# Optimization experiments

Hardware: AMD Instinct MI355X
Metric: run time of the kernel (lower is better)

Reference implementation:

```python
import jax, jax.numpy as jnp
import numpy as np

# Constants mirroring MS / MultiLayers_MS forward args (scalars closed over)
HEADS = 8
BETA = 0.5          # GAT_MS_2_3 init arg 'beta' (mean-shift coordinate gate strength)
T = 1.0             # temperature 't' forward arg
BAND_WIDTH = 1.0    # 'band_width' forward arg
MAX_ITER = 3        # 'max_iter' forward arg (iterative mean-shift steps)
SELF_DISTANCE = 0.01  # 'self_distance' forward arg: distance assigned to the diagonal
USE_STD_ATT = False # 'use_std_att' forward arg
NEG_INF = -1e9


def setup_inputs() -> dict:
    key = jax.random.key(0)
    ks = jax.random.split(key, 16)
    N, D = 3072, 256
    x = jax.random.normal(ks[0], (N, D), dtype=jnp.float32)
    xyz = jax.random.normal(ks[1], (N, 3), dtype=jnp.float32) * 3.0
    # delta_y = |y_hat - y_hat^T| as produced by GAT_Classifier (detached)
    y_hat = jax.random.uniform(ks[2], (N, 1), dtype=jnp.float32)
    delta_y = jnp.abs(y_hat - y_hat.T)
    distance_mask = jax.random.uniform(ks[3], (N, N)) < 0.3   # sparse pairwise gate
    big_inter_mask = jax.random.uniform(ks[4], (N, N)) < 0.9  # inter-chain gate
    s = 1.0 / np.sqrt(D)  # ~ xavier_uniform scale for D x D
    def lin_w(k):
        return jax.random.uniform(k, (D, D), jnp.float32, minval=-s, maxval=s)
    Wq, Wk, Wv, Wo = lin_w(ks[5]), lin_w(ks[6]), lin_w(ks[7]), lin_w(ks[8])
    z = jnp.zeros((D,), jnp.float32)
    return dict(x=x, xyz=xyz, delta_y=delta_y,
                distance_mask=distance_mask, big_inter_mask=big_inter_mask,
                Wq=Wq, bq=z, Wk=Wk, bk=z, Wv=Wv, bv=z, Wo=Wo, bo=z)


def _mean_shift(xyz, q, k, v, delta_y, valid):
    """Iterative distance/band-masked multi-head attention (mean_shift).
    q,k,v: [N,H,Dh]; delta_y: [N,N]; valid: [N,N] bool. Returns (xyz, feat [N,D])."""
    N, H, Dh = q.shape
    eye = jnp.eye(N, dtype=bool)
    # content scores, computed once (q,k fixed across iterations)
    scores = jnp.einsum('nhd,mhd->hnm', q, k) / jnp.sqrt(jnp.float32(Dh))  # [H,N,N]
    if USE_STD_ATT:
        mu = scores.mean(axis=-1, keepdims=True)
        sd = scores.std(axis=-1, keepdims=True)
        scores = (scores - mu) / (sd + 1e-5)
    inv2bw2 = 1.0 / (2.0 * BAND_WIDTH * BAND_WIDTH)
    feat = None
    for _ in range(MAX_ITER):
        # pairwise squared distances of current coordinates [N,N]
        d2 = jnp.sum((xyz[:, None, :] - xyz[None, :, :]) ** 2, axis=-1)
        d2 = jnp.where(eye, SELF_DISTANCE ** 2, d2)
        # banded logits: content score, Gaussian distance band, prediction-difference gate
        logits = T * scores - BETA * (d2 * inv2bw2) - delta_y  # [H,N,N]
        logits = jnp.where(valid, logits, NEG_INF)
        attn = jax.nn.softmax(logits, axis=-1)                 # [H,N,N]
        xyz = attn.mean(axis=0) @ xyz                          # mean-shift coords [N,3]
        feat = jnp.einsum('hnm,mhd->nhd', attn, v).reshape(N, H * Dh)
    return xyz, feat


def reference(x, xyz, delta_y, distance_mask, big_inter_mask,
              Wq, bq, Wk, bk, Wv, bv, Wo, bo):
    N, D = x.shape
    H, Dh = HEADS, D // HEADS
    q = (x @ Wq + bq).reshape(N, H, Dh)
    k = (x @ Wk + bk).reshape(N, H, Dh)
    v = (x @ Wv + bv).reshape(N, H, Dh)
    eye = jnp.eye(N, dtype=bool)
    valid = (distance_mask & big_inter_mask) | eye  # keep self to avoid empty rows
    xyz_out, feat = _mean_shift(xyz, q, k, v, delta_y, valid)
    out = feat @ Wo + bo + x   # out_proj + residual (MS.forward)
    return xyz_out, out
```

## Files before the change

### kernel.cpp

```cpp
#include <hip/hip_runtime.h>
#include <hip/hip_fp16.h>

#define NN 3072
#define DD 256
#define NH 8
#define SPLIT 4
#define KT (NN / SPLIT / 64)
#define NKT2 (NN / 64)
#define VHALF ((NN / 16) * 256)
#define LN2INV 1.4426950408889634f

typedef _Float16 h16;
typedef __attribute__((ext_vector_type(4))) _Float16 half4;
typedef __attribute__((ext_vector_type(8))) _Float16 half8;
typedef __attribute__((ext_vector_type(4))) float f32x4;

#if __has_builtin(__builtin_amdgcn_exp2f)
#define EXP2(x) __builtin_amdgcn_exp2f(x)
#else
#define EXP2(x) __expf((x) * 0.69314718056f)
#endif

#define MFMA16(a, b, c) __builtin_amdgcn_mfma_f32_16x16x16f16(a, b, c, 0, 0, 0)

__device__ __forceinline__ void async16(const h16* g, h16* l, int lane) {
#if __has_builtin(__builtin_amdgcn_global_load_lds)
  __builtin_amdgcn_global_load_lds(
      (const __attribute__((address_space(1))) void*)(g + (size_t)lane * 8),
      (__attribute__((address_space(3))) void*)l, 16, 0, 0);
#else
  *(half8*)(l + lane * 8) = *(const half8*)(g + (size_t)lane * 8);
#endif
}

__device__ inline void write_aug(int q, float x, float y, float z,
                                 h16* __restrict__ qaug, h16* __restrict__ kaug,
                                 h16* __restrict__ xzT3) {
  float sx = 0.5f * LN2INV * x, sy = 0.5f * LN2INV * y, sz = 0.5f * LN2INV * z;
  h16 shx = (h16)sx, shy = (h16)sy, shz = (h16)sz;
  h16 slx = (h16)(sx - (float)shx), sly = (h16)(sy - (float)shy), slz = (h16)(sz - (float)shz);
  h16 hx = (h16)x, hy = (h16)y, hz = (h16)z;
  h16 lx = (h16)(x - (float)hx), ly = (h16)(y - (float)hy), lz = (h16)(z - (float)hz);
  float n2n = -0.25f * LN2INV * (x * x + y * y + z * z);
  h16 nh = (h16)n2n, nl = (h16)(n2n - (float)nh);
  h16 qa[16], ka[16];
  #pragma unroll
  for (int i = 0; i < 16; ++i) { qa[i] = (h16)0.f; ka[i] = (h16)0.f; }
  qa[0] = shx; qa[1] = shy; qa[2] = shz;
  qa[3] = shx; qa[4] = shy; qa[5] = shz;
  qa[6] = slx; qa[7] = sly; qa[8] = slz;
  qa[9] = (h16)1.f; qa[10] = (h16)1.f;
  qa[11] = (h16)n2n;
  ka[0] = hx; ka[1] = hy; ka[2] = hz;
  ka[3] = lx; ka[4] = ly; ka[5] = lz;
  ka[6] = hx; ka[7] = hy; ka[8] = hz;
  ka[9] = nh; ka[10] = nl;
  ka[11] = (h16)1.f;
  *(half8*)(qaug + (size_t)q * 16) = ((half8*)qa)[0];
  *(half8*)(qaug + (size_t)q * 16 + 8) = ((half8*)qa)[1];
  *(half8*)(kaug + (size_t)q * 16) = ((half8*)ka)[0];
  *(half8*)(kaug + (size_t)q * 16 + 8) = ((half8*)ka)[1];
  int kt2 = q >> 6, kk = q & 63;
  int f = kk >> 4, qd = (kk >> 2) & 3, j = kk & 3;
  h16* b = xzT3 + ((size_t)kt2 << 10) + f * 256 + qd * 64 + j;
  b[0] = (h16)1.f;
  b[4] = hx; b[8] = hy; b[12] = hz;
  b[16] = lx; b[20] = ly; b[24] = lz;
  #pragma unroll
  for (int m = 7; m < 16; ++m) b[m * 4] = (h16)0.f;
}

__global__ __launch_bounds__(256) void k_convert(
    const float* __restrict__ x, const float* __restrict__ xyz,
    h16* __restrict__ xb, h16* __restrict__ qaug,
    h16* __restrict__ kaug, h16* __restrict__ xzT3,
    float* __restrict__ numT) {
  int t = blockIdx.x * 256 + threadIdx.x;
  const int NX = NN * DD;
  if (t < NX) { xb[t] = (h16)x[t]; numT[t] = 0.f; return; }
  int q = t - NX;
  if (q < NN) write_aug(q, xyz[q * 3], xyz[q * 3 + 1], xyz[q * 3 + 2], qaug, kaug, xzT3);
}

__global__ __launch_bounds__(256) void k_wt(
    const float* __restrict__ Wq, const float* __restrict__ Wk,
    const float* __restrict__ Wv, const float* __restrict__ Wo,
    h16* __restrict__ wtq, h16* __restrict__ wtk, h16* __restrict__ wtv,
    h16* __restrict__ wto) {
  __shared__ float tile[32][33];
  int m = blockIdx.z;
  const float* W = (m == 0) ? Wq : (m == 1) ? Wk : (m == 2) ? Wv : Wo;
  h16* wt = (m == 0) ? wtq : (m == 1) ? wtk : (m == 2) ? wtv : wto;
  int n0 = blockIdx.x * 32, k0 = blockIdx.y * 32;
  int tx = threadIdx.x & 31, ty = threadIdx.x >> 5;
  #pragma unroll
  for (int i = 0; i < 4; ++i)
    tile[ty + i * 8][tx] = W[(size_t)(k0 + ty + i * 8) * 256 + n0 + tx];
  __syncthreads();
  #pragma unroll
  for (int i = 0; i < 4; ++i)
    wt[(size_t)(n0 + ty + i * 8) * 256 + k0 + tx] = (h16)tile[tx][ty + i * 8];
}

__global__ __launch_bounds__(256) void k_prep(
    const float* __restrict__ dy, const int* __restrict__ dm,
    const int* __restrict__ bim, h16* __restrict__ dynT3) {
  __shared__ h16 sv[16][1036];
  int qt = blockIdx.y;
  int cb = blockIdx.x;
  int t = threadIdx.x;
  int c0 = cb * 1024 + t * 4;
  #pragma unroll
  for (int r = 0; r < 16; ++r) {
    int row = qt * 16 + r;
    size_t idx = (size_t)row * NN + c0;
    int4 m4 = *(const int4*)(dm + idx);
    int4 b4 = *(const int4*)(bim + idx);
    float4 d4 = *(const float4*)(dy + idx);
    h16* s = &sv[r][t * 4];
    int mm[4] = {m4.x & b4.x, m4.y & b4.y, m4.z & b4.z, m4.w & b4.w};
    float dd[4] = {d4.x, d4.y, d4.z, d4.w};
    #pragma unroll
    for (int j = 0; j < 4; ++j) {
      bool diag = (row == c0 + j);
      bool valid = (mm[j] != 0) | diag;
      s[j] = (h16)(valid ? (-LN2INV * (dd[j] + (diag ? 2.5e-5f : 0.f))) : -43281.f);
    }
  }
  __syncthreads();
  #pragma unroll
  for (int s2 = 0; s2 < 8; ++s2) {
    int s = t + s2 * 256;
    int tile = s >> 7;
    int sl = s & 127;
    int chunk = sl >> 6;
    int lane = sl & 63;
    int row = lane & 15, quad = lane >> 4;
    int base = tile * 64 + chunk * 32 + quad * 4;
    half4 lo = *(const half4*)&sv[row][base];
    half4 hi = *(const half4*)&sv[row][base + 16];
    half8 o;
    #pragma unroll
    for (int j = 0; j < 4; ++j) { o[j] = lo[j]; o[j + 4] = hi[j]; }
    h16* dst = dynT3 + (((size_t)qt * NKT2 + (cb * 16 + tile)) << 10) + sl * 8;
    *(half8*)dst = o;
  }
}

__device__ inline void gemm_body(const h16* __restrict__ A, const h16* __restrict__ Bt,
                                 const float* __restrict__ bias, void* __restrict__ out,
                                 const float* __restrict__ resid, int M, int mode,
                                 float scale, int bx, int by) {
  int lane = threadIdx.x & 63;
  int wave = threadIdx.x >> 6;
  int col = lane & 15, quad = lane >> 4;
  int m0 = bx * 32;
  int n0 = by * 64 + wave * 16;
  f32x4 acc[2];
  acc[0] = (f32x4){0.f, 0.f, 0.f, 0.f};
  acc[1] = (f32x4){0.f, 0.f, 0.f, 0.f};
  #pragma unroll
  for (int kk = 0; kk < DD; kk += 32) {
    half8 b = *(const half8*)(Bt + (size_t)(n0 + col) * DD + kk + quad * 8);
    #pragma unroll
    for (int mr = 0; mr < 2; ++mr) {
      half8 a = *(const half8*)(A + (size_t)(m0 + mr * 16 + col) * DD + kk + quad * 8);
      acc[mr] = __builtin_amdgcn_mfma_f32_16x16x32_f16(a, b, acc[mr], 0, 0, 0);
    }
  }
  float bb = bias[n0 + col];
  #pragma unroll
  for (int mr = 0; mr < 2; ++mr) {
    #pragma unroll
    for (int r = 0; r < 4; ++r) {
      int m = m0 + mr * 16 + quad * 4 + r;
      int n = n0 + col;
      float v = acc[mr][r] + bb;
      if (mode == 0)      ((h16*)out)[(size_t)m * DD + n] = (h16)(v * scale);
      else if (mode == 3) ((h16*)out)[((size_t)(n >> 5) * NN + m) * 32 + (n & 31)] = (h16)v;
      else if (mode == 4) {
        int hh = n >> 5, d = n & 31;
        size_t a = ((((size_t)hh * 2 + (d >> 4)) * (NN / 16) + (m >> 4)) * 64 +
                    ((m >> 2) & 3) * 16 + (d & 15)) * 4 + (m & 3);
        ((h16*)out)[a] = (h16)v;
      }
      else ((float*)out)[(size_t)m * DD + n] = v + resid[(size_t)m * DD + n];
    }
  }
}

__global__ __launch_bounds__(256) void k_gemm(
    const h16* __restrict__ A, const h16* __restrict__ Bt,
    const float* __restrict__ bias, void* __restrict__ out,
    const float* __restrict__ resid, int M, int mode, float scale) {
  gemm_body(A, Bt, bias, out, resid, M, mode, scale, blockIdx.x, blockIdx.y);
}

__global__ __launch_bounds__(256) void k_gemm3(
    const h16* __restrict__ A, const h16* __restrict__ wtq,
    const h16* __restrict__ wtk, const h16* __restrict__ wtv,
    const float* __restrict__ bq, const float* __restrict__ bk,
    const float* __restrict__ bv, h16* __restrict__ qb, h16* __restrict__ kbh,
    h16* __restrict__ vA, float qscale) {
  int z = blockIdx.z;
  const h16* Bt = (z == 0) ? wtq : (z == 1) ? wtk : wtv;
  const float* bias = (z == 0) ? bq : (z == 1) ? bk : bv;
  void* out = (z == 0) ? (void*)qb : (z == 1) ? (void*)kbh : (void*)vA;
  int mode = (z == 0) ? 0 : (z == 1) ? 3 : 4;
  gemm_body(A, Bt, bias, out, nullptr, NN, mode, (z == 0) ? qscale : 1.f,
            blockIdx.x, blockIdx.y);
}

__device__ __forceinline__ void stage_tile(int h, int lane, int qt, int kt2,
                                           const h16* __restrict__ dynT3,
                                           const h16* __restrict__ kaug,
                                           const h16* __restrict__ xzT3,
                                           h16* bdy, h16* bka, h16* bxz) {
  if (h < 2)
    async16(dynT3 + (((size_t)qt * NKT2 + kt2) << 10) + h * 512, bdy + h * 512, lane);
  else if (h < 4)
    async16(kaug + ((size_t)kt2 << 10) + (h - 2) * 512, bka + (h - 2) * 512, lane);
  else if (h < 6)
    async16(xzT3 + ((size_t)kt2 << 10) + (h - 4) * 512, bxz + (h - 4) * 512, lane);
}

__device__ __forceinline__ void ldkf(const h16* __restrict__ kbh_h, int k0,
                                     int col, int quad, half8 kf[4]) {
  #pragma unroll
  for (int f = 0; f < 4; ++f)
    kf[f] = *(const half8*)(kbh_h + (size_t)(k0 + f * 16 + col) * 32 + quad * 8);
}

template <int LAST>
__device__ __forceinline__ void ms_compute(
    const h16* __restrict__ bdy, const h16* __restrict__ bka,
    const h16* __restrict__ bxz, const half8 kf[4], half8 qaf, half8 qf,
    const h16* __restrict__ vA0, int lane, int col, int quad,
    f32x4& accS, f32x4& fc0, f32x4& fc1) {
  half8 kz = {};
  half8 dv0 = *(const half8*)(bdy + lane * 8);
  half8 dv1 = *(const half8*)(bdy + 512 + lane * 8);
  #pragma unroll
  for (int f = 0; f < 4; ++f) {
    half8 ka = (quad < 2) ? *(const half8*)(bka + (f * 16 + col) * 16 + quad * 8) : kz;
    half8 dv = (f & 2) ? dv1 : dv0;
    f32x4 cc;
    #pragma unroll
    for (int r = 0; r < 4; ++r) cc[r] = (float)dv[(f & 1) * 4 + r];
    f32x4 g = __builtin_amdgcn_mfma_f32_16x16x32_f16(ka, qaf, cc, 0, 0, 0);
    f32x4 s = __builtin_amdgcn_mfma_f32_16x16x32_f16(kf[f], qf, g, 0, 0, 0);
    half4 pv;
    #pragma unroll
    for (int r = 0; r < 4; ++r) pv[r] = (h16)EXP2(s[r]);
    half4 xa = *(const half4*)(bxz + f * 256 + lane * 4);
    accS = MFMA16(xa, pv, accS);
    if (LAST) {
      half4 v0 = *(const half4*)(vA0 + f * 256 + lane * 4);
      half4 v1 = *(const half4*)(vA0 + VHALF + f * 256 + lane * 4);
      fc0 = MFMA16(v0, pv, fc0);
      fc1 = MFMA16(v1, pv, fc1);
    }
  }
}

template <int LAST>
__global__ __launch_bounds__(512, 4) void k_msattn(
    const h16* __restrict__ qb, const h16* __restrict__ kbh,
    const h16* __restrict__ vA, const h16* __restrict__ dynT3,
    const h16* __restrict__ qaug, const h16* __restrict__ kaug,
    const h16* __restrict__ xzT3, float* __restrict__ den_s,
    float* __restrict__ axh_s, float* __restrict__ axl_s,
    float* __restrict__ numT) {
  __shared__ h16 s_dy[2][1024];
  __shared__ h16 s_ka[2][1024];
  __shared__ h16 s_xz[2][1024];
  const int tid = threadIdx.x;
  const int h = tid >> 6;
  const int lane = tid & 63;
  const int col = lane & 15;
  const int quad = lane >> 4;
  const int qt = blockIdx.x;
  const int q0 = qt * 16;
  const int tb = blockIdx.y * KT;

  half8 kz = {};
  half8 qf = *(const half8*)(qb + (size_t)(q0 + col) * DD + h * 32 + quad * 8);
  half8 qaf = (quad < 2) ? *(const half8*)(qaug + (size_t)(q0 + col) * 16 + quad * 8) : kz;
  const h16* kbh_h = kbh + (size_t)h * NN * 32;
  const h16* vb = vA + (size_t)h * 2 * (NN / 16) * 256;
  f32x4 accS = (f32x4){0.f, 0.f, 0.f, 0.f};
  f32x4 fc0 = (f32x4){0.f, 0.f, 0.f, 0.f};
  f32x4 fc1 = (f32x4){0.f, 0.f, 0.f, 0.f};
  half8 kfA[4], kfB[4];

  stage_tile(h, lane, qt, tb, dynT3, kaug, xzT3, s_dy[0], s_ka[0], s_xz[0]);
  ldkf(kbh_h, tb * 64, col, quad, kfA);
  __syncthreads();
  #pragma unroll 1
  for (int kt = 0; kt < KT; kt += 2) {
    int t1 = tb + kt + 1;
    stage_tile(h, lane, qt, t1, dynT3, kaug, xzT3, s_dy[1], s_ka[1], s_xz[1]);
    ldkf(kbh_h, t1 * 64, col, quad, kfB);
    ms_compute<LAST>(s_dy[0], s_ka[0], s_xz[0], kfA, qaf, qf,
                     vb + (size_t)(tb + kt) * 1024,
                     lane, col, quad, accS, fc0, fc1);
    __syncthreads();
    int t2 = (kt + 2 < KT) ? tb + kt + 2 : t1;
    if (kt + 2 < KT)
      stage_tile(h, lane, qt, t2, dynT3, kaug, xzT3, s_dy[0], s_ka[0], s_xz[0]);
    ldkf(kbh_h, t2 * 64, col, quad, kfA);
    ms_compute<LAST>(s_dy[1], s_ka[1], s_xz[1], kfB, qaf, qf,
                     vb + (size_t)t1 * 1024,
                     lane, col, quad, accS, fc0, fc1);
    __syncthreads();
  }

  int q = q0 + col;
  size_t sidx = (size_t)(blockIdx.y * NH + h) * NN + q;
  if (quad == 0) {
    den_s[sidx] = accS[0];
    axh_s[sidx * 3 + 0] = accS[1];
    axh_s[sidx * 3 + 1] = accS[2];
    axh_s[sidx * 3 + 2] = accS[3];
  } else if (quad == 1) {
    axl_s[sidx * 3 + 0] = accS[0];
    axl_s[sidx * 3 + 1] = accS[1];
    axl_s[sidx * 3 + 2] = accS[2];
  }
  if (LAST) {
    #pragma unroll
    for (int r = 0; r < 4; ++r) {
      atomicAdd(&numT[(size_t)(h * 32 + quad * 4 + r) * NN + q], fc0[r]);
      atomicAdd(&numT[(size_t)(h * 32 + 16 + quad * 4 + r) * NN + q], fc1[r]);
    }
  }
}

__global__ __launch_bounds__(256) void k_combine(
    const float* __restrict__ den_s, const float* __restrict__ axh_s,
    const float* __restrict__ axl_s, float* __restrict__ den_tot,
    h16* __restrict__ qaug, h16* __restrict__ kaug, h16* __restrict__ xzT3,
    float* __restrict__ out3) {
  int h = threadIdx.x & 7;
  int q = blockIdx.x * 32 + (threadIdx.x >> 3);
  float d = 0.f, x = 0.f, y = 0.f, z = 0.f;
  #pragma unroll
  for (int s = 0; s < SPLIT; ++s) {
    size_t idx = (size_t)(s * NH + h) * NN + q;
    d += den_s[idx];
    x += axh_s[idx * 3 + 0] + axl_s[idx * 3 + 0];
    y += axh_s[idx * 3 + 1] + axl_s[idx * 3 + 1];
    z += axh_s[idx * 3 + 2] + axl_s[idx * 3 + 2];
  }
  den_tot[h * NN + q] = d;
  float inv = 0.125f / d;
  float X = x * inv, Y = y * inv, Z = z * inv;
  #pragma unroll
  for (int m = 1; m < 8; m <<= 1) {
    X += __shfl_xor(X, m);
    Y += __shfl_xor(Y, m);
    Z += __shfl_xor(Z, m);
  }
  if (h == 0) {
    if (out3) {
      out3[q * 3 + 0] = X;
      out3[q * 3 + 1] = Y;
      out3[q * 3 + 2] = Z;
    } else {
      write_aug(q, X, Y, Z, qaug, kaug, xzT3);
    }
  }
}

__global__ __launch_bounds__(256) void k_finish(
    const float* __restrict__ numT, const float* __restrict__ den_tot,
    h16* __restrict__ featb) {
  __shared__ float tile[32][33];
  int q0 = blockIdx.x * 32, d0 = blockIdx.y * 32;
  int tx = threadIdx.x & 31, ty = threadIdx.x >> 5;
  #pragma unroll
  for (int i = 0; i < 4; ++i)
    tile[ty + i * 8][tx] = numT[(size_t)(d0 + ty + i * 8) * NN + q0 + tx];
  __syncthreads();
  int h = d0 >> 5;
  #pragma unroll
  for (int i = 0; i < 4; ++i) {
    int q = q0 + ty + i * 8;
    float inv = 1.f / den_tot[h * NN + q];
    featb[(size_t)q * DD + d0 + tx] = (h16)(tile[tx][ty + i * 8] * inv);
  }
}

extern "C" void kernel_launch(void* const* d_in, const int* in_sizes, int n_in,
                              void* d_out, int out_size, void* d_ws, size_t ws_size,
                              hipStream_t stream) {
  const float* x   = (const float*)d_in[0];
  const float* xyz = (const float*)d_in[1];
  const float* dy  = (const float*)d_in[2];
  const int* dm    = (const int*)d_in[3];
  const int* bim   = (const int*)d_in[4];
  const float* Wq = (const float*)d_in[5];
  const float* bq = (const float*)d_in[6];
  const float* Wk = (const float*)d_in[7];
  const float* bk = (const float*)d_in[8];
  const float* Wv = (const float*)d_in[9];
  const float* bv = (const float*)d_in[10];
  const float* Wo = (const float*)d_in[11];
  const float* bo = (const float*)d_in[12];

  char* p = (char*)d_ws;
  h16* xb  = (h16*)p; p += (size_t)NN * DD * 2;
  h16* wtq = (h16*)p; p += 256 * 256 * 2;
  h16* wtk = (h16*)p; p += 256 * 256 * 2;
  h16* wtv = (h16*)p; p += 256 * 256 * 2;
  h16* wto = (h16*)p; p += 256 * 256 * 2;
  h16* qb    = (h16*)p; p += (size_t)NN * DD * 2;
  h16* kbh   = (h16*)p; p += (size_t)NN * DD * 2;
  h16* vA    = (h16*)p; p += (size_t)NN * DD * 2;
  h16* featb = (h16*)p; p += (size_t)NN * DD * 2;
  h16* dynT3 = (h16*)p; p += (size_t)NN * NN * 2;
  h16* qaug  = (h16*)p; p += (size_t)NN * 16 * 2;
  h16* kaug  = (h16*)p; p += (size_t)NN * 16 * 2;
  h16* xzT3  = (h16*)p; p += (size_t)NKT2 * 1024 * 2;
  float* den_s = (float*)p; p += (size_t)SPLIT * NH * NN * 4;
  float* axh_s = (float*)p; p += (size_t)SPLIT * NH * NN * 3 * 4;
  float* axl_s = (float*)p; p += (size_t)SPLIT * NH * NN * 3 * 4;
  float* den_tot = (float*)p; p += (size_t)NH * NN * 4;
  float* numT = (float*)p; p += (size_t)DD * NN * 4;

  k_convert<<<(NN * DD + NN + 255) / 256, 256, 0, stream>>>(x, xyz, xb, qaug,
                                                            kaug, xzT3, numT);
  k_wt<<<dim3(8, 8, 4), 256, 0, stream>>>(Wq, Wk, Wv, Wo, wtq, wtk, wtv, wto);
  k_prep<<<dim3(3, 192), 256, 0, stream>>>(dy, dm, bim, dynT3);
  k_gemm3<<<dim3(96, 4, 3), 256, 0, stream>>>(xb, wtq, wtk, wtv, bq, bk, bv,
                                              qb, kbh, vA,
                                              0.17677669529663689f * LN2INV);

  float* xyz_final = (float*)d_out;
  float* out_final = (float*)d_out + NN * 3;

  k_msattn<0><<<dim3(NN / 16, SPLIT), 512, 0, stream>>>(
      qb, kbh, vA, dynT3, qaug, kaug, xzT3, den_s, axh_s, axl_s, nullptr);
  k_combine<<<96, 256, 0, stream>>>(den_s, axh_s, axl_s, den_tot,
                                    qaug, kaug, xzT3, nullptr);
  k_msattn<0><<<dim3(NN / 16, SPLIT), 512, 0, stream>>>(
      qb, kbh, vA, dynT3, qaug, kaug, xzT3, den_s, axh_s, axl_s, nullptr);
  k_combine<<<96, 256, 0, stream>>>(den_s, axh_s, axl_s, den_tot,
                                    qaug, kaug, xzT3, nullptr);
  k_msattn<1><<<dim3(NN / 16, SPLIT), 512, 0, stream>>>(
      qb, kbh, vA, dynT3, qaug, kaug, xzT3, den_s, axh_s, axl_s, numT);
  k_combine<<<96, 256, 0, stream>>>(den_s, axh_s, axl_s, den_tot,
                                    nullptr, nullptr, nullptr, xyz_final);
  k_finish<<<dim3(96, 8), 256, 0, stream>>>(numT, den_tot, featb);
  k_gemm<<<dim3(96, 4), 256, 0, stream>>>(featb, wto, bo, out_final, x, NN, 2, 1.f);
}
```

Baseline: 320.3 us.

## Merge preprocessing kernels into one launch and stagger attention block start

Fuses the three preprocessing kernels (fp16 conversion/aug setup, weight transposes, mask/delta packing) into a single launch that dispatches on block index range, cutting two kernel launches and their gaps. It also makes each attention block sleep in proportion to its linear block index divided by 256, staggering when blocks start. The staggering is meant to spread out the memory traffic at kernel start, but it delays later blocks and may add idle time.

```diff
diff --git a/kernel.cpp b/kernel.cpp
--- a/kernel.cpp
+++ b/kernel.cpp
@@ -9,6 +9,9 @@
 #define NKT2 (NN / 64)
 #define VHALF ((NN / 16) * 256)
 #define LN2INV 1.4426950408889634f
+#define PREP_BLKS 576
+#define CONV_BLKS ((NN * DD + NN) / 256)
+#define WT_BLKS 256
 
 typedef _Float16 h16;
 typedef __attribute__((ext_vector_type(4))) _Float16 half4;
@@ -70,80 +73,78 @@
   for (int m = 7; m < 16; ++m) b[m * 4] = (h16)0.f;
 }
 
-__global__ __launch_bounds__(256) void k_convert(
+__global__ __launch_bounds__(256) void k_pre(
     const float* __restrict__ x, const float* __restrict__ xyz,
-    h16* __restrict__ xb, h16* __restrict__ qaug,
-    h16* __restrict__ kaug, h16* __restrict__ xzT3,
-    float* __restrict__ numT) {
-  int t = blockIdx.x * 256 + threadIdx.x;
-  const int NX = NN * DD;
-  if (t < NX) { xb[t] = (h16)x[t]; numT[t] = 0.f; return; }
-  int q = t - NX;
-  if (q < NN) write_aug(q, xyz[q * 3], xyz[q * 3 + 1], xyz[q * 3 + 2], qaug, kaug, xzT3);
-}
-
-__global__ __launch_bounds__(256) void k_wt(
+    const float* __restrict__ dy, const int* __restrict__ dm,
+    const int* __restrict__ bim,
     const float* __restrict__ Wq, const float* __restrict__ Wk,
     const float* __restrict__ Wv, const float* __restrict__ Wo,
+    h16* __restrict__ xb, h16* __restrict__ qaug, h16* __restrict__ kaug,
+    h16* __restrict__ xzT3, float* __restrict__ numT,
     h16* __restrict__ wtq, h16* __restrict__ wtk, h16* __restrict__ wtv,
-    h16* __restrict__ wto) {
-  __shared__ float tile[32][33];
-  int m = blockIdx.z;
-  const float* W = (m == 0) ? Wq : (m == 1) ? Wk : (m == 2) ? Wv : Wo;
-  h16* wt = (m == 0) ? wtq : (m == 1) ? wtk : (m == 2) ? wtv : wto;
-  int n0 = blockIdx.x * 32, k0 = blockIdx.y * 32;
-  int tx = threadIdx.x & 31, ty = threadIdx.x >> 5;
-  #pragma unroll
-  for (int i = 0; i < 4; ++i)
-    tile[ty + i * 8][tx] = W[(size_t)(k0 + ty + i * 8) * 256 + n0 + tx];
-  __syncthreads();
-  #pragma unroll
-  for (int i = 0; i < 4; ++i)
-    wt[(size_t)(n0 + ty + i * 8) * 256 + k0 + tx] = (h16)tile[tx][ty + i * 8];
-}
-
-__global__ __launch_bounds__(256) void k_prep(
-    const float* __restrict__ dy, const int* __restrict__ dm,
-    const int* __restrict__ bim, h16* __restrict__ dynT3) {
+    h16* __restrict__ wto, h16* __restrict__ dynT3) {
   __shared__ h16 sv[16][1036];
-  int qt = blockIdx.y;
-  int cb = blockIdx.x;
+  int b = blockIdx.x;
   int t = threadIdx.x;
-  int c0 = cb * 1024 + t * 4;
-  #pragma unroll
-  for (int r = 0; r < 16; ++r) {
-    int row = qt * 16 + r;
-    size_t idx = (size_t)row * NN + c0;
-    int4 m4 = *(const int4*)(dm + idx);
-    int4 b4 = *(const int4*)(bim + idx);
-    float4 d4 = *(const float4*)(dy + idx);
-    h16* s = &sv[r][t * 4];
-    int mm[4] = {m4.x & b4.x, m4.y & b4.y, m4.z & b4.z, m4.w & b4.w};
-    float dd[4] = {d4.x, d4.y, d4.z, d4.w};
-    #pragma unroll
-    for (int j = 0; j < 4; ++j) {
-      bool diag = (row == c0 + j);
-      bool valid = (mm[j] != 0) | diag;
-      s[j] = (h16)(valid ? (-LN2INV * (dd[j] + (diag ? 2.5e-5f : 0.f))) : -43281.f);
-    }
-  }
-  __syncthreads();
-  #pragma unroll
-  for (int s2 = 0; s2 < 8; ++s2) {
-    int s = t + s2 * 256;
-    int tile = s >> 7;
-    int sl = s & 127;
-    int chunk = sl >> 6;
-    int lane = sl & 63;
-    int row = lane & 15, quad = lane >> 4;
-    int base = tile * 64 + chunk * 32 + quad * 4;
-    half4 lo = *(const half4*)&sv[row][base];
-    half4 hi = *(const half4*)&sv[row][base + 16];
-    half8 o;
-    #pragma unroll
-    for (int j = 0; j < 4; ++j) { o[j] = lo[j]; o[j + 4] = hi[j]; }
-    h16* dst = dynT3 + (((size_t)qt * NKT2 + (cb * 16 + tile)) << 10) + sl * 8;
-    *(half8*)dst = o;
+  if (b < PREP_BLKS) {
+    int cb = b % 3, qt = b / 3;
+    int c0 = cb * 1024 + t * 4;
+    #pragma unroll
+    for (int r = 0; r < 16; ++r) {
+      int row = qt * 16 + r;
+      size_t idx = (size_t)row * NN + c0;
+      int4 m4 = *(const int4*)(dm + idx);
+      int4 b4 = *(const int4*)(bim + idx);
+      float4 d4 = *(const float4*)(dy + idx);
+      h16* s = &sv[r][t * 4];
+      int mm[4] = {m4.x & b4.x, m4.y & b4.y, m4.z & b4.z, m4.w & b4.w};
+      float dd[4] = {d4.x, d4.y, d4.z, d4.w};
+      #pragma unroll
+      for (int j = 0; j < 4; ++j) {
+        bool diag = (row == c0 + j);
+        bool valid = (mm[j] != 0) | diag;
+        s[j] = (h16)(valid ? (-LN2INV * (dd[j] + (diag ? 2.5e-5f : 0.f))) : -43281.f);
+      }
+    }
+    __syncthreads();
+    #pragma unroll
+    for (int s2 = 0; s2 < 8; ++s2) {
+      int s = t + s2 * 256;
+      int tile = s >> 7;
+      int sl = s & 127;
+      int lane = sl & 63;
+      int row = lane & 15, quad = lane >> 4;
+      int base = tile * 64 + (sl >> 6) * 32 + quad * 4;
+      half4 lo = *(const half4*)&sv[row][base];
+      half4 hi = *(const half4*)&sv[row][base + 16];
+      half8 o;
+      #pragma unroll
+      for (int j = 0; j < 4; ++j) { o[j] = lo[j]; o[j + 4] = hi[j]; }
+      h16* dst = dynT3 + (((size_t)qt * NKT2 + (cb * 16 + tile)) << 10) + sl * 8;
+      *(half8*)dst = o;
+    }
+  } else if (b < PREP_BLKS + CONV_BLKS) {
+    int u = (b - PREP_BLKS) * 256 + t;
+    const int NX = NN * DD;
+    if (u < NX) { xb[u] = (h16)x[u]; numT[u] = 0.f; return; }
+    int q = u - NX;
+    if (q < NN)
+      write_aug(q, xyz[q * 3], xyz[q * 3 + 1], xyz[q * 3 + 2], qaug, kaug, xzT3);
+  } else {
+    float* tf = (float*)sv;
+    int w = b - PREP_BLKS - CONV_BLKS;
+    int m = w >> 6;
+    int n0 = (w & 7) * 32, k0 = ((w >> 3) & 7) * 32;
+    const float* W = (m == 0) ? Wq : (m == 1) ? Wk : (m == 2) ? Wv : Wo;
+    h16* wt = (m == 0) ? wtq : (m == 1) ? wtk : (m == 2) ? wtv : wto;
+    int tx = t & 31, ty = t >> 5;
+    #pragma unroll
+    for (int i = 0; i < 4; ++i)
+      tf[(ty + i * 8) * 33 + tx] = W[(size_t)(k0 + ty + i * 8) * 256 + n0 + tx];
+    __syncthreads();
+    #pragma unroll
+    for (int i = 0; i < 4; ++i)
+      wt[(size_t)(n0 + ty + i * 8) * 256 + k0 + tx] = (h16)tf[tx * 33 + ty + i * 8];
   }
 }
 
@@ -282,6 +283,12 @@
   const int qt = blockIdx.x;
   const int q0 = qt * 16;
   const int tb = blockIdx.y * KT;
+
+  int phase = (blockIdx.x + gridDim.x * blockIdx.y) >> 8;
+  for (int i = 0; i < phase; ++i) {
+    __builtin_amdgcn_s_sleep(16);
+    __builtin_amdgcn_s_sleep(16);
+  }
 
   half8 kz = {};
   half8 qf = *(const half8*)(qb + (size_t)(q0 + col) * DD + h * 32 + quad * 8);
@@ -428,10 +435,9 @@
   float* den_tot = (float*)p; p += (size_t)NH * NN * 4;
   float* numT = (float*)p; p += (size_t)DD * NN * 4;
 
-  k_convert<<<(NN * DD + NN + 255) / 256, 256, 0, stream>>>(x, xyz, xb, qaug,
-                                                            kaug, xzT3, numT);
-  k_wt<<<dim3(8, 8, 4), 256, 0, stream>>>(Wq, Wk, Wv, Wo, wtq, wtk, wtv, wto);
-  k_prep<<<dim3(3, 192), 256, 0, stream>>>(dy, dm, bim, dynT3);
+  k_pre<<<PREP_BLKS + CONV_BLKS + WT_BLKS, 256, 0, stream>>>(
+      x, xyz, dy, dm, bim, Wq, Wk, Wv, Wo,
+      xb, qaug, kaug, xzT3, numT, wtq, wtk, wtv, wto, dynT3);
   k_gemm3<<<dim3(96, 4, 3), 256, 0, stream>>>(xb, wtq, wtk, wtv, bq, bk, bv,
                                               qb, kbh, vA,
                                               0.17677669529663689f * LN2INV);
```

Measured after the change: 312.4 us. -2.5%, faster.
